# Performance work log

Hardware: AMD Instinct MI355X
Metric: run time of the kernel (lower is better)

## Reference

```python
import jax, jax.numpy as jnp
import numpy as np

B, D, H, E, NDIFF = 4096, 2048, 4096, 8, 3
TOPK = 2


def setup_inputs() -> dict:
    key = jax.random.key(0)
    ks = jax.random.split(key, 8)
    x = jax.random.normal(ks[0], (B, D), dtype=jnp.float32)
    difficulty_labels = jax.random.randint(ks[1], (B,), 0, NDIFF)
    emb = jax.random.normal(ks[2], (NDIFF, D), dtype=jnp.float32) * 0.02
    gate_W = jax.random.normal(ks[3], (E, 2 * D), dtype=jnp.float32) / np.sqrt(2.0 * D)
    gate_b = jnp.zeros((E,), dtype=jnp.float32)
    expert_W = jax.random.normal(ks[4], (E, H, D), dtype=jnp.float32) / np.sqrt(D)
    expert_b = jax.random.normal(ks[5], (E, H), dtype=jnp.float32) * 0.01
    return {"x": x, "difficulty_labels": difficulty_labels, "emb": emb,
            "gate_W": gate_W, "gate_b": gate_b,
            "expert_W": expert_W, "expert_b": expert_b}


def reference(x, difficulty_labels, emb, gate_W, gate_b, expert_W, expert_b):
    # gating: concat token features with difficulty embedding
    gate_in = jnp.concatenate([x, emb[difficulty_labels]], axis=1)       # [B, 2D]
    gate_logits = gate_in @ gate_W.T + gate_b                             # [B, E]
    topw, topk_idx = jax.lax.top_k(gate_logits, TOPK)                     # [B, 2]
    topk_probs = jax.nn.softmax(topw, axis=1)                             # [B, 2]
    # per-token combine weight for each expert (top-2 indices are distinct)
    combine = jnp.zeros((x.shape[0], E), dtype=x.dtype)
    combine = combine.at[jnp.arange(x.shape[0])[:, None], topk_idx].add(topk_probs)
    # dispatch/compute/combine: tokens with combine weight 0 contribute 0,
    # matching the masked gather/scatter-add of the original.
    out = jnp.zeros((x.shape[0], expert_W.shape[1]), dtype=x.dtype)
    for e in range(E):  # small fixed loop over experts
        y = x @ expert_W[e].T + expert_b[e]                               # [B, H]
        out = out + y * combine[:, e:e + 1]
    return (out, topk_idx)
```

## Files before the change

### kernel.cpp

```cpp
#include <hip/hip_runtime.h>
#include <hip/hip_bf16.h>

#define B_TOK 4096
#define DIM   2048
#define HID   4096
#define NEXP  8
#define CAP   4224

#define BM 128
#define BN 128
#define BK 64
#define LSTRIDE 72

typedef short  bf16x8 __attribute__((ext_vector_type(8)));
typedef unsigned short us16x8 __attribute__((ext_vector_type(8)));
typedef float  f32x4  __attribute__((ext_vector_type(4)));

__device__ __forceinline__ unsigned short f2bf(float f) {
    unsigned u = __builtin_bit_cast(unsigned, f);
    u += 0x7fffu + ((u >> 16) & 1u);
    return (unsigned short)(u >> 16);
}

__global__ __launch_bounds__(256) void compute_c_kernel(
    const float* __restrict__ emb, const float* __restrict__ gate_W,
    const float* __restrict__ gate_b, float* __restrict__ cbuf) {
    int wave = (blockIdx.x * blockDim.x + threadIdx.x) >> 6;
    int lane = threadIdx.x & 63;
    if (wave >= 24) return;
    int n = wave >> 3, e = wave & 7;
    const float4* er = (const float4*)(emb + (size_t)n * DIM);
    const float4* wr = (const float4*)(gate_W + (size_t)e * 2 * DIM + DIM);
    float acc = 0.f;
    for (int c = lane; c < DIM / 4; c += 64) {
        float4 a = er[c], b = wr[c];
        acc += a.x * b.x + a.y * b.y + a.z * b.z + a.w * b.w;
    }
    #pragma unroll
    for (int off = 32; off; off >>= 1) acc += __shfl_down(acc, off, 64);
    if (lane == 0) cbuf[n * 8 + e] = acc + gate_b[e];
}

__global__ __launch_bounds__(256) void gating_kernel(
    const float* __restrict__ x, const int* __restrict__ labels,
    const float* __restrict__ gate_W, const float* __restrict__ cbuf,
    int* __restrict__ counts, int* __restrict__ tlist,
    float* __restrict__ wlist, float* __restrict__ out_idx) {
    int wave = threadIdx.x >> 6, lane = threadIdx.x & 63;
    int b = blockIdx.x * 4 + wave;
    const float4* xr  = (const float4*)(x + (size_t)b * DIM);
    const float4* gw4 = (const float4*)gate_W;
    float acc[8] = {0.f, 0.f, 0.f, 0.f, 0.f, 0.f, 0.f, 0.f};
    for (int c = lane; c < DIM / 4; c += 64) {
        float4 xv = xr[c];
        #pragma unroll
        for (int e = 0; e < 8; ++e) {
            float4 wv = gw4[e * (2 * DIM / 4) + c];
            acc[e] += xv.x * wv.x + xv.y * wv.y + xv.z * wv.z + xv.w * wv.w;
        }
    }
    #pragma unroll
    for (int off = 32; off; off >>= 1) {
        #pragma unroll
        for (int e = 0; e < 8; ++e) acc[e] += __shfl_down(acc[e], off, 64);
    }
    if (lane == 0) {
        int lbl = labels[b];
        float lg[8];
        #pragma unroll
        for (int e = 0; e < 8; ++e) lg[e] = acc[e] + cbuf[lbl * 8 + e];
        int e0 = 0; float t0 = lg[0];
        #pragma unroll
        for (int e = 1; e < 8; ++e) if (lg[e] > t0) { t0 = lg[e]; e0 = e; }
        int e1 = -1; float t1 = -1e30f;
        #pragma unroll
        for (int e = 0; e < 8; ++e)
            if (e != e0 && lg[e] > t1) { t1 = lg[e]; e1 = e; }
        float w0 = 1.f / (1.f + expf(t1 - t0));
        float w1 = 1.f - w0;
        int p0 = atomicAdd(&counts[e0], 1);
        tlist[e0 * CAP + p0] = b; wlist[e0 * CAP + p0] = w0;
        int p1 = atomicAdd(&counts[e1], 1);
        tlist[e1 * CAP + p1] = b; wlist[e1 * CAP + p1] = w1;
        out_idx[2 * b]     = (float)e0;
        out_idx[2 * b + 1] = (float)e1;
    }
}

__global__ void pad_kernel(const int* __restrict__ counts,
                           int* __restrict__ tlist, float* __restrict__ wlist) {
    int e = blockIdx.x, c = counts[e];
    int padded = (c + BM - 1) & ~(BM - 1);
    int i = c + threadIdx.x;
    if (i < padded) { tlist[e * CAP + i] = 0; wlist[e * CAP + i] = 0.f; }
}

__global__ __launch_bounds__(256) void moe_gemm_kernel(
    const float* __restrict__ x, const float* __restrict__ expert_W,
    const float* __restrict__ expert_b, const int* __restrict__ counts,
    const int* __restrict__ tlist, const float* __restrict__ wlist,
    float* __restrict__ out) {
    const int e  = blockIdx.z;
    const int m0 = blockIdx.y * BM;
    if (m0 >= counts[e]) return;
    const int n0 = blockIdx.x * BN;

    __shared__ unsigned short As[BM][LSTRIDE];
    __shared__ unsigned short Bs[BN][LSTRIDE];
    __shared__ int   toks[BM];
    __shared__ float wts[BM];

    const int t = threadIdx.x;
    if (t < BM) {
        toks[t] = tlist[e * CAP + m0 + t];
        wts[t]  = wlist[e * CAP + m0 + t];
    }
    __syncthreads();

    const int lane = t & 63, wave = t >> 6;
    const int wm = wave >> 1, wn = wave & 1;
    const int r = lane & 15, quad = lane >> 4;
    const float* Wbase = expert_W + (size_t)e * HID * DIM;

    f32x4 acc[4][4] = {};

    const int srow = t >> 3;
    const int scol = (t & 7) * 8;

    for (int k0 = 0; k0 < DIM; k0 += BK) {
        #pragma unroll
        for (int rr = 0; rr < 4; ++rr) {
            int row = srow + rr * 32;
            const float* src = x + (size_t)toks[row] * DIM + k0 + scol;
            float4 v0 = *(const float4*)src;
            float4 v1 = *(const float4*)(src + 4);
            us16x8 o = { f2bf(v0.x), f2bf(v0.y), f2bf(v0.z), f2bf(v0.w),
                         f2bf(v1.x), f2bf(v1.y), f2bf(v1.z), f2bf(v1.w) };
            *(us16x8*)&As[row][scol] = o;
        }
        #pragma unroll
        for (int rr = 0; rr < 4; ++rr) {
            int row = srow + rr * 32;
            const float* src = Wbase + (size_t)(n0 + row) * DIM + k0 + scol;
            float4 v0 = *(const float4*)src;
            float4 v1 = *(const float4*)(src + 4);
            us16x8 o = { f2bf(v0.x), f2bf(v0.y), f2bf(v0.z), f2bf(v0.w),
                         f2bf(v1.x), f2bf(v1.y), f2bf(v1.z), f2bf(v1.w) };
            *(us16x8*)&Bs[row][scol] = o;
        }
        __syncthreads();
        #pragma unroll
        for (int kk = 0; kk < 2; ++kk) {
            bf16x8 af[4], bfr[4];
            #pragma unroll
            for (int i = 0; i < 4; ++i) {
                af[i]  = *(const bf16x8*)&As[wm * 64 + i * 16 + r][kk * 32 + quad * 8];
                bfr[i] = *(const bf16x8*)&Bs[wn * 64 + i * 16 + r][kk * 32 + quad * 8];
            }
            #pragma unroll
            for (int im = 0; im < 4; ++im)
                #pragma unroll
                for (int in = 0; in < 4; ++in)
                    acc[im][in] = __builtin_amdgcn_mfma_f32_16x16x32_bf16(
                        af[im], bfr[in], acc[im][in], 0, 0, 0);
        }
        __syncthreads();
    }

    const float* eb = expert_b + (size_t)e * HID;
    #pragma unroll
    for (int in = 0; in < 4; ++in) {
        int col = n0 + wn * 64 + in * 16 + r;
        float bias = eb[col];
        #pragma unroll
        for (int im = 0; im < 4; ++im) {
            int rowb = wm * 64 + im * 16 + quad * 4;
            #pragma unroll
            for (int r4 = 0; r4 < 4; ++r4) {
                int row = rowb + r4;
                float w = wts[row];
                if (w != 0.f)
                    atomicAdd(out + (size_t)toks[row] * HID + col,
                              w * (acc[im][in][r4] + bias));
            }
        }
    }
}

extern "C" void kernel_launch(void* const* d_in, const int* in_sizes, int n_in,
                              void* d_out, int out_size, void* d_ws, size_t ws_size,
                              hipStream_t stream) {
    const float* x        = (const float*)d_in[0];
    const int*   labels   = (const int*)  d_in[1];
    const float* emb      = (const float*)d_in[2];
    const float* gate_W   = (const float*)d_in[3];
    const float* gate_b   = (const float*)d_in[4];
    const float* expert_W = (const float*)d_in[5];
    const float* expert_b = (const float*)d_in[6];
    float* out = (float*)d_out;

    char* ws = (char*)d_ws;
    int*   counts = (int*)ws;
    float* cbuf   = (float*)(ws + 128);
    int*   tlist  = (int*)(ws + 512);
    float* wlist  = (float*)(ws + 512 + NEXP * CAP * 4);

    hipMemsetAsync(counts, 0, 8 * sizeof(int), stream);
    hipMemsetAsync(out, 0, (size_t)B_TOK * HID * sizeof(float), stream);

    compute_c_kernel<<<6, 256, 0, stream>>>(emb, gate_W, gate_b, cbuf);
    gating_kernel<<<B_TOK / 4, 256, 0, stream>>>(
        x, labels, gate_W, cbuf, counts, tlist, wlist,
        out + (size_t)B_TOK * HID);
    pad_kernel<<<NEXP, BM, 0, stream>>>(counts, tlist, wlist);
    moe_gemm_kernel<<<dim3(HID / BN, B_TOK / BM, NEXP), 256, 0, stream>>>(
        x, expert_W, expert_b, counts, tlist, wlist, out);
}
```

Before: 893.2 us.

## Pre-convert inputs to bf16 and stream tiles via direct global-to-LDS loads

Adds conversion kernels that turn x and all expert weights into bf16 buffers in the workspace before the GEMM. The GEMM then loads tiles with global_load_lds async copies into an XOR-swizzled unpadded LDS layout, instead of loading fp32, converting in registers and storing to padded shared memory. The aim is to halve GEMM global traffic and remove per-tile conversion work. In exchange there is an extra full pass over the 256MB of expert weights every call, and the load is still not double-buffered. It also switches gating to a fast exp and reorders the atomics.

```diff
diff --git a/kernel.cpp b/kernel.cpp
--- a/kernel.cpp
+++ b/kernel.cpp
@@ -10,7 +10,6 @@
 #define BM 128
 #define BN 128
 #define BK 64
-#define LSTRIDE 72
 
 typedef short  bf16x8 __attribute__((ext_vector_type(8)));
 typedef unsigned short us16x8 __attribute__((ext_vector_type(8)));
@@ -20,6 +19,23 @@
     unsigned u = __builtin_bit_cast(unsigned, f);
     u += 0x7fffu + ((u >> 16) & 1u);
     return (unsigned short)(u >> 16);
+}
+
+__device__ __forceinline__ void async_copy16(const void* g, void* l) {
+    __builtin_amdgcn_global_load_lds(
+        (const __attribute__((address_space(1))) unsigned*)g,
+        (__attribute__((address_space(3))) unsigned*)l, 16, 0, 0);
+}
+
+__global__ __launch_bounds__(256) void cvt_kernel(
+    const float* __restrict__ src, unsigned short* __restrict__ dst, long n) {
+    long i = ((long)blockIdx.x * 256 + threadIdx.x) * 8;
+    if (i >= n) return;
+    float4 v0 = *(const float4*)(src + i);
+    float4 v1 = *(const float4*)(src + i + 4);
+    us16x8 o = { f2bf(v0.x), f2bf(v0.y), f2bf(v0.z), f2bf(v0.w),
+                 f2bf(v1.x), f2bf(v1.y), f2bf(v1.z), f2bf(v1.w) };
+    *(us16x8*)(dst + i) = o;
 }
 
 __global__ __launch_bounds__(256) void compute_c_kernel(
@@ -76,11 +92,11 @@
         #pragma unroll
         for (int e = 0; e < 8; ++e)
             if (e != e0 && lg[e] > t1) { t1 = lg[e]; e1 = e; }
-        float w0 = 1.f / (1.f + expf(t1 - t0));
+        float w0 = 1.f / (1.f + __expf(t1 - t0));
         float w1 = 1.f - w0;
         int p0 = atomicAdd(&counts[e0], 1);
+        int p1 = atomicAdd(&counts[e1], 1);
         tlist[e0 * CAP + p0] = b; wlist[e0 * CAP + p0] = w0;
-        int p1 = atomicAdd(&counts[e1], 1);
         tlist[e1 * CAP + p1] = b; wlist[e1 * CAP + p1] = w1;
         out_idx[2 * b]     = (float)e0;
         out_idx[2 * b + 1] = (float)e1;
@@ -96,7 +112,7 @@
 }
 
 __global__ __launch_bounds__(256) void moe_gemm_kernel(
-    const float* __restrict__ x, const float* __restrict__ expert_W,
+    const unsigned short* __restrict__ xb, const unsigned short* __restrict__ Wb,
     const float* __restrict__ expert_b, const int* __restrict__ counts,
     const int* __restrict__ tlist, const float* __restrict__ wlist,
     float* __restrict__ out) {
@@ -105,8 +121,8 @@
     if (m0 >= counts[e]) return;
     const int n0 = blockIdx.x * BN;
 
-    __shared__ unsigned short As[BM][LSTRIDE];
-    __shared__ unsigned short Bs[BN][LSTRIDE];
+    __shared__ unsigned short As[BM * BK];
+    __shared__ unsigned short Bs[BN * BK];
     __shared__ int   toks[BM];
     __shared__ float wts[BM];
 
@@ -118,44 +134,41 @@
     __syncthreads();
 
     const int lane = t & 63, wave = t >> 6;
+    const int rowc = lane >> 3;
+    const int gsw  = ((lane & 7) ^ rowc) * 8;
+
+    const unsigned short* gA[4];
+    const unsigned short* gB[4];
+    unsigned short* ldsA[4];
+    unsigned short* ldsB[4];
+    #pragma unroll
+    for (int j = 0; j < 4; ++j) {
+        int row = wave * 32 + j * 8 + rowc;
+        gA[j] = xb + (size_t)toks[row] * DIM + gsw;
+        gB[j] = Wb + ((size_t)e * HID + n0 + row) * DIM + gsw;
+        ldsA[j] = As + (wave * 32 + j * 8) * BK;
+        ldsB[j] = Bs + (wave * 32 + j * 8) * BK;
+    }
+
     const int wm = wave >> 1, wn = wave & 1;
     const int r = lane & 15, quad = lane >> 4;
-    const float* Wbase = expert_W + (size_t)e * HID * DIM;
 
     f32x4 acc[4][4] = {};
 
-    const int srow = t >> 3;
-    const int scol = (t & 7) * 8;
-
     for (int k0 = 0; k0 < DIM; k0 += BK) {
         #pragma unroll
-        for (int rr = 0; rr < 4; ++rr) {
-            int row = srow + rr * 32;
-            const float* src = x + (size_t)toks[row] * DIM + k0 + scol;
-            float4 v0 = *(const float4*)src;
-            float4 v1 = *(const float4*)(src + 4);
-            us16x8 o = { f2bf(v0.x), f2bf(v0.y), f2bf(v0.z), f2bf(v0.w),
-                         f2bf(v1.x), f2bf(v1.y), f2bf(v1.z), f2bf(v1.w) };
-            *(us16x8*)&As[row][scol] = o;
-        }
-        #pragma unroll
-        for (int rr = 0; rr < 4; ++rr) {
-            int row = srow + rr * 32;
-            const float* src = Wbase + (size_t)(n0 + row) * DIM + k0 + scol;
-            float4 v0 = *(const float4*)src;
-            float4 v1 = *(const float4*)(src + 4);
-            us16x8 o = { f2bf(v0.x), f2bf(v0.y), f2bf(v0.z), f2bf(v0.w),
-                         f2bf(v1.x), f2bf(v1.y), f2bf(v1.z), f2bf(v1.w) };
-            *(us16x8*)&Bs[row][scol] = o;
-        }
+        for (int j = 0; j < 4; ++j) async_copy16(gA[j] + k0, ldsA[j]);
+        #pragma unroll
+        for (int j = 0; j < 4; ++j) async_copy16(gB[j] + k0, ldsB[j]);
         __syncthreads();
         #pragma unroll
         for (int kk = 0; kk < 2; ++kk) {
             bf16x8 af[4], bfr[4];
+            const int pg = ((kk * 4 + quad) ^ (r & 7)) * 8;
             #pragma unroll
             for (int i = 0; i < 4; ++i) {
-                af[i]  = *(const bf16x8*)&As[wm * 64 + i * 16 + r][kk * 32 + quad * 8];
-                bfr[i] = *(const bf16x8*)&Bs[wn * 64 + i * 16 + r][kk * 32 + quad * 8];
+                af[i]  = *(const bf16x8*)&As[(wm * 64 + i * 16 + r) * BK + pg];
+                bfr[i] = *(const bf16x8*)&Bs[(wn * 64 + i * 16 + r) * BK + pg];
             }
             #pragma unroll
             for (int im = 0; im < 4; ++im)
@@ -204,15 +217,21 @@
     float* cbuf   = (float*)(ws + 128);
     int*   tlist  = (int*)(ws + 512);
     float* wlist  = (float*)(ws + 512 + NEXP * CAP * 4);
+    unsigned short* xb = (unsigned short*)(ws + 512 + 2 * NEXP * CAP * 4);
+    unsigned short* Wb = xb + (size_t)B_TOK * DIM;
 
     hipMemsetAsync(counts, 0, 8 * sizeof(int), stream);
     hipMemsetAsync(out, 0, (size_t)B_TOK * HID * sizeof(float), stream);
 
+    cvt_kernel<<<(B_TOK * DIM) / (8 * 256), 256, 0, stream>>>(
+        x, xb, (long)B_TOK * DIM);
+    cvt_kernel<<<(NEXP * HID * DIM) / (8 * 256), 256, 0, stream>>>(
+        expert_W, Wb, (long)NEXP * HID * DIM);
     compute_c_kernel<<<6, 256, 0, stream>>>(emb, gate_W, gate_b, cbuf);
     gating_kernel<<<B_TOK / 4, 256, 0, stream>>>(
         x, labels, gate_W, cbuf, counts, tlist, wlist,
         out + (size_t)B_TOK * HID);
     pad_kernel<<<NEXP, BM, 0, stream>>>(counts, tlist, wlist);
     moe_gemm_kernel<<<dim3(HID / BN, B_TOK / BM, NEXP), 256, 0, stream>>>(
-        x, expert_W, expert_b, counts, tlist, wlist, out);
-}
+        xb, Wb, expert_b, counts, tlist, wlist, out);
+}
```

After: 891.5 us. No clear change (-0.2%).
